# Optimization experiments

Measured on AMD Instinct MI355X. Metric: run time of the kernel, lower is better.

Reference implementation:

```python
import jax, jax.numpy as jnp
import numpy as np

# Winograd F(4x4, 3x3) transform matrices (wincnn convention, as in jiecaoyu/winograd)
BT = jnp.array([
    [4.,  0., -5.,  0., 1., 0.],
    [0., -4., -4.,  1., 1., 0.],
    [0.,  4., -4., -1., 1., 0.],
    [0., -2., -1.,  2., 1., 0.],
    [0.,  2., -1., -2., 1., 0.],
    [0.,  4.,  0., -5., 0., 1.]], dtype=jnp.float32)  # [6,6]
AT = jnp.array([
    [1., 1.,  1., 1.,  1., 0.],
    [0., 1., -1., 2., -2., 0.],
    [0., 1.,  1., 4.,  4., 0.],
    [0., 1., -1., 8., -8., 1.]], dtype=jnp.float32)  # [4,6]

KERNEL = 3
PAD = 1
GROUPS = 1
TILE_IN = 6   # input_tile_size
TILE_OUT = 4  # output_tile_size


def setup_inputs() -> dict:
    key = jax.random.key(0)
    k1, k2, k3 = jax.random.split(key, 3)
    N, Cin, H, W = 16, 64, 128, 128
    Cout = 64
    x = jax.random.normal(k1, (N, Cin, H, W), dtype=jnp.float32)
    # weight is stored in the Winograd (6x6 spectral) domain, as in the module
    weight = jax.random.normal(k2, (Cout, Cin // GROUPS, TILE_IN, TILE_IN), dtype=jnp.float32) * 0.01
    bias = jax.random.normal(k3, (Cout,), dtype=jnp.float32) * 0.01
    return {"x": x, "weight": weight, "bias": bias}


def reference(x, weight, bias):
    N, Cin, H0, W0 = x.shape
    Cout = weight.shape[0]
    g = GROUPS
    # conv padding
    x = jnp.pad(x, ((0, 0), (0, 0), (PAD, PAD), (PAD, PAD)))
    H = x.shape[2]
    out_w = H - KERNEL + 1
    # pad so output width is a multiple of the output tile size
    extra = (-out_w) % TILE_OUT
    if extra:
        x = jnp.pad(x, ((0, 0), (0, 0), (0, extra), (0, extra)))
    nt = (x.shape[2] - TILE_IN) // TILE_OUT + 1  # tiles per spatial dim
    # extract overlapping 6x6 tiles with stride 4 (the torch unfold)
    idx = jnp.arange(nt)[:, None] * TILE_OUT + jnp.arange(TILE_IN)[None, :]  # [nt,6]
    tiles = x[:, :, idx]                 # [N,C,nt,6,Wp]
    tiles = tiles[:, :, :, :, idx]       # [N,C,nt,6,nt,6]
    # input transform: V = BT @ d @ BT^T per tile -> [N,C,nt,nt,6,6]
    V = jnp.einsum('ai,ncpiqj,bj->ncpqab', BT, tiles, BT)
    # grouped spectral GEMM over input channels
    Vg = V.reshape(N, g, Cin // g, nt, nt, TILE_IN, TILE_IN)
    Wg = weight.reshape(g, Cout // g, Cin // g, TILE_IN, TILE_IN)
    M = jnp.einsum('goiab,ngipqab->ngopqab', Wg, Vg)
    M = M.reshape(N, Cout, nt, nt, TILE_IN, TILE_IN)
    # output transform: Y = AT @ M @ AT^T per tile -> [N,O,nt,nt,4,4]
    Y = jnp.einsum('xa,nopqab,yb->nopqxy', AT, M, AT)
    # stitch tiles back: [N,O,nt,4,nt,4] -> [N,O,nt*4,nt*4]
    y = Y.transpose(0, 1, 2, 4, 3, 5).reshape(N, Cout, nt * TILE_OUT, nt * TILE_OUT)
    y = y + bias[None, :, None, None]
    # crop the extra padding
    y = y[:, :, :out_w, :out_w]
    return y
```

## Files before the change

kernel.cpp:

```cpp
#include <hip/hip_runtime.h>
#include <stdint.h>

typedef __attribute__((ext_vector_type(4))) float f32x4;
typedef __attribute__((ext_vector_type(8))) short s16x8;

#define WB_BYTES 294912

__device__ __forceinline__ short f2bf(float f) {
    uint32_t u = __builtin_bit_cast(uint32_t, f);
    u = u + 0x7FFFu + ((u >> 16) & 1u);
    return (short)(u >> 16);
}

__global__ __launch_bounds__(256) void wtrans(const float* __restrict__ wf, short* __restrict__ wb) {
    int tid = blockIdx.x * 256 + threadIdx.x;
    const float* src = wf + tid * 36;
    float w[36];
#pragma unroll
    for (int i = 0; i < 9; i++) {
        f32x4 v = *(const f32x4*)(src + 4 * i);
        w[4*i+0] = v[0]; w[4*i+1] = v[1]; w[4*i+2] = v[2]; w[4*i+3] = v[3];
    }
#pragma unroll
    for (int ab = 0; ab < 36; ab++) wb[ab * 4096 + tid] = f2bf(w[ab]);
}

#define XS 343
__global__ __launch_bounds__(1024) void wino_fused(const float* __restrict__ x,
                                                   const short* __restrict__ wb,
                                                   const float* __restrict__ bias,
                                                   float* __restrict__ out) {
    __shared__ __align__(16) float SM[32768];
    float* X = SM;
    short* Vs = (short*)(SM + 32 * XS);
    float* P0 = SM;
    float* P1 = SM + 16384;

    int t = threadIdx.x;
    int lane = t & 63;
    int w = t >> 6;
    int cog = w >> 2;
    int grp = w & 3;
    int sh = grp >> 1;
    int bh = grp & 1;
    int lo = lane & 15;
    int kq = lane >> 4;

    int b = blockIdx.x;
    int n = b >> 6;
    int sb = b & 63;
    int p0_ = (sb >> 3) * 4;
    int q0_ = (sb & 7) * 4;
    const float* xb = x + (size_t)n * 64 * 16384;
    int row0 = 4 * p0_ - 1;
    int col0a = 4 * q0_ - 4;

    int ci_t = t & 31;
    int tl_t = (t >> 5) & 15;
    int s2_t = t >> 9;
    int tp = tl_t >> 2, tq = tl_t & 3;

    f32x4 acc[9];
#pragma unroll
    for (int i = 0; i < 9; i++) acc[i] = (f32x4){0.f, 0.f, 0.f, 0.f};

#pragma unroll
    for (int r = 0; r < 2; r++) {
#pragma unroll
        for (int i = 0; i < 4; i++) {
            int s = i * 1024 + t;
            if (s < 3456) {
                int cis = s / 108;
                int rs = s - cis * 108;
                int row = rs / 6;
                int c4 = rs - row * 6;
                int gr = row0 + row;
                int gc = col0a + 4 * c4;
                float v0 = 0.f, v1 = 0.f, v2 = 0.f, v3 = 0.f;
                if ((unsigned)gr < 128u) {
                    const float* rowp = xb + (size_t)((r * 32 + cis) * 128 + gr) * 128;
                    if (gc >= 0 && gc + 3 < 128) {
                        f32x4 v = *(const f32x4*)(rowp + gc);
                        v0 = v[0]; v1 = v[1]; v2 = v[2]; v3 = v[3];
                    } else {
                        if ((unsigned)(gc + 0) < 128u) v0 = rowp[gc + 0];
                        if ((unsigned)(gc + 1) < 128u) v1 = rowp[gc + 1];
                        if ((unsigned)(gc + 2) < 128u) v2 = rowp[gc + 2];
                        if ((unsigned)(gc + 3) < 128u) v3 = rowp[gc + 3];
                    }
                }
                int base = cis * XS + row * 18;
                int cl = 4 * c4 - 3;
                if ((unsigned)(cl + 0) < 18u) X[base + cl + 0] = v0;
                if ((unsigned)(cl + 1) < 18u) X[base + cl + 1] = v1;
                if ((unsigned)(cl + 2) < 18u) X[base + cl + 2] = v2;
                if ((unsigned)(cl + 3) < 18u) X[base + cl + 3] = v3;
            }
        }
        __syncthreads();

        {
            const float* Xb = X + ci_t * XS + (4 * tp) * 18 + 4 * tq;
            float Ua[3][6];
#pragma unroll
            for (int c = 0; c < 6; c++) {
                if (s2_t == 0) {
                    float m0 = Xb[0 * 18 + c], m1 = Xb[1 * 18 + c], m2 = Xb[2 * 18 + c];
                    float m3 = Xb[3 * 18 + c], m4 = Xb[4 * 18 + c];
                    float e = fmaf(-4.f, m2, m4);
                    float f = fmaf(-4.f, m1, m3);
                    Ua[0][c] = fmaf(4.f, m0 - m2, m4 - m2);
                    Ua[1][c] = e + f;
                    Ua[2][c] = e - f;
                } else {
                    float m1 = Xb[1 * 18 + c], m2 = Xb[2 * 18 + c];
                    float m3 = Xb[3 * 18 + c], m4 = Xb[4 * 18 + c], m5 = Xb[5 * 18 + c];
                    float g = m4 - m2, h = m3 - m1;
                    Ua[0][c] = fmaf(2.f, h, g);
                    Ua[1][c] = fmaf(-2.f, h, g);
                    Ua[2][c] = fmaf(4.f, m1 - m3, m5 - m3);
                }
            }
            short* vb = Vs + tl_t * 32 + ci_t;
#pragma unroll
            for (int ar = 0; ar < 3; ar++) {
                float m0 = Ua[ar][0], m1 = Ua[ar][1], m2 = Ua[ar][2];
                float m3 = Ua[ar][3], m4 = Ua[ar][4], m5 = Ua[ar][5];
                float e = fmaf(-4.f, m2, m4);
                float f = fmaf(-4.f, m1, m3);
                float g = m4 - m2;
                float h = m3 - m1;
                int abb = (s2_t * 3 + ar) * 6;
                vb[(abb + 0) * 512] = f2bf(fmaf(4.f, m0 - m2, g));
                vb[(abb + 1) * 512] = f2bf(e + f);
                vb[(abb + 2) * 512] = f2bf(e - f);
                vb[(abb + 3) * 512] = f2bf(fmaf(2.f, h, g));
                vb[(abb + 4) * 512] = f2bf(fmaf(-2.f, h, g));
                vb[(abb + 5) * 512] = f2bf(fmaf(4.f, m1 - m3, m5 - m3));
            }
        }
        __syncthreads();

        {
            const short* wb_base = wb + (cog * 16 + lo) * 64 + r * 32 + kq * 8;
            const short* v_base = Vs + lo * 32 + kq * 8;
#pragma unroll
            for (int ar = 0; ar < 3; ar++) {
#pragma unroll
                for (int br = 0; br < 3; br++) {
                    int ab = (3 * sh + ar) * 6 + (3 * bh + br);
                    s16x8 a0 = *(const s16x8*)(wb_base + ab * 4096);
                    s16x8 b0 = *(const s16x8*)(v_base + ab * 512);
                    acc[ar * 3 + br] = __builtin_amdgcn_mfma_f32_16x16x32_bf16(a0, b0, acc[ar * 3 + br], 0, 0, 0);
                }
            }
        }
    }

    __syncthreads();
    int p = p0_ + (lo >> 2);
    int q = q0_ + (lo & 3);
    float* Pown = (sh == 0) ? P0 : P1;

    if (bh == 0) {
#pragma unroll
        for (int rr = 0; rr < 4; rr++) {
            float z[4][3];
#pragma unroll
            for (int br = 0; br < 3; br++) {
                float ma = acc[br][rr], mb = acc[3 + br][rr], mc = acc[6 + br][rr];
                if (sh == 0) {
                    float s1 = mb + mc, d1 = mb - mc;
                    z[0][br] = ma + s1; z[1][br] = d1; z[2][br] = s1; z[3][br] = d1;
                } else {
                    float sv = ma + mb, dv = ma - mb;
                    z[0][br] = sv; z[1][br] = 2.f * dv; z[2][br] = 4.f * sv;
                    z[3][br] = fmaf(8.f, dv, mc);
                }
            }
#pragma unroll
            for (int xr = 0; xr < 4; xr++) {
                float s1 = z[xr][1] + z[xr][2], d1 = z[xr][1] - z[xr][2];
                f32x4 y;
                y[0] = z[xr][0] + s1; y[1] = d1; y[2] = s1; y[3] = d1;
                *(f32x4*)&Pown[cog * 4096 + (rr * 4 + xr) * 256 + lane * 4] = y;
            }
        }
    }
    __syncthreads();
    if (bh == 1) {
#pragma unroll
        for (int rr = 0; rr < 4; rr++) {
            float z[4][3];
#pragma unroll
            for (int br = 0; br < 3; br++) {
                float ma = acc[br][rr], mb = acc[3 + br][rr], mc = acc[6 + br][rr];
                if (sh == 0) {
                    float s1 = mb + mc, d1 = mb - mc;
                    z[0][br] = ma + s1; z[1][br] = d1; z[2][br] = s1; z[3][br] = d1;
                } else {
                    float sv = ma + mb, dv = ma - mb;
                    z[0][br] = sv; z[1][br] = 2.f * dv; z[2][br] = 4.f * sv;
                    z[3][br] = fmaf(8.f, dv, mc);
                }
            }
#pragma unroll
            for (int xr = 0; xr < 4; xr++) {
                float s2 = z[xr][0] + z[xr][1], d2 = z[xr][0] - z[xr][1];
                f32x4 y;
                y[0] = s2; y[1] = 2.f * d2; y[2] = 4.f * s2;
                y[3] = fmaf(8.f, d2, z[xr][2]);
                float* pp = &Pown[cog * 4096 + (rr * 4 + xr) * 256 + lane * 4];
                f32x4 old = *(const f32x4*)pp;
                *(f32x4*)pp = old + y;
            }
        }
    }
    __syncthreads();
    {
        int rr = grp;
        int co = cog * 16 + kq * 4 + rr;
        float bv = bias[co];
        float* ob = out + ((size_t)(n * 64 + co) * 128 + 4 * p) * 128 + 4 * q;
#pragma unroll
        for (int xr = 0; xr < 4; xr++) {
            int idx = cog * 4096 + (rr * 4 + xr) * 256 + lane * 4;
            f32x4 a0 = *(const f32x4*)&P0[idx];
            f32x4 a1 = *(const f32x4*)&P1[idx];
            f32x4 y;
            y[0] = a0[0] + a1[0] + bv;
            y[1] = a0[1] + a1[1] + bv;
            y[2] = a0[2] + a1[2] + bv;
            y[3] = a0[3] + a1[3] + bv;
            *(f32x4*)(ob + xr * 128) = y;
        }
    }
}

extern "C" void kernel_launch(void* const* d_in, const int* in_sizes, int n_in,
                              void* d_out, int out_size, void* d_ws, size_t ws_size,
                              hipStream_t stream) {
    const float* x    = (const float*)d_in[0];
    const float* wf   = (const float*)d_in[1];
    const float* bias = (const float*)d_in[2];
    float* out = (float*)d_out;

    if (ws_size < WB_BYTES) return;
    short* wb = (short*)d_ws;

    wtrans<<<16, 256, 0, stream>>>(wf, wb);
    wino_fused<<<1024, 1024, 0, stream>>>(x, wb, bias, out);
}
```

Before: 185.9 us.

## Make Winograd kernel persistent over four tiles with register-prefetched input loads

After: 224.1 us. +20.6%, slower.

```diff
diff --git a/kernel.cpp b/kernel.cpp
--- a/kernel.cpp
+++ b/kernel.cpp
@@ -2,6 +2,7 @@
 #include <stdint.h>
 
 typedef __attribute__((ext_vector_type(4))) float f32x4;
+typedef __attribute__((ext_vector_type(2))) float f32x2;
 typedef __attribute__((ext_vector_type(8))) short s16x8;
 
 #define WB_BYTES 294912
@@ -12,6 +13,12 @@
     return (short)(u >> 16);
 }
 
+__device__ __forceinline__ f32x4 load4u(const float* p) {
+    f32x4 v;
+    __builtin_memcpy(&v, p, 16);
+    return v;
+}
+
 __global__ __launch_bounds__(256) void wtrans(const float* __restrict__ wf, short* __restrict__ wb) {
     int tid = blockIdx.x * 256 + threadIdx.x;
     const float* src = wf + tid * 36;
@@ -25,14 +32,15 @@
     for (int ab = 0; ab < 36; ab++) wb[ab * 4096 + tid] = f2bf(w[ab]);
 }
 
-#define XS 343
+#define XCI 440
 __global__ __launch_bounds__(1024) void wino_fused(const float* __restrict__ x,
                                                    const short* __restrict__ wb,
                                                    const float* __restrict__ bias,
                                                    float* __restrict__ out) {
-    __shared__ __align__(16) float SM[32768];
-    float* X = SM;
-    short* Vs = (short*)(SM + 32 * XS);
+    __shared__ __align__(16) float SM[39680];
+    float* X0 = SM;
+    float* X1 = SM + 14080;
+    short* Vs = (short*)(SM + 28160);
     float* P0 = SM;
     float* P1 = SM + 16384;
 
@@ -46,194 +54,233 @@
     int lo = lane & 15;
     int kq = lane >> 4;
 
-    int b = blockIdx.x;
-    int n = b >> 6;
-    int sb = b & 63;
-    int p0_ = (sb >> 3) * 4;
-    int q0_ = (sb & 7) * 4;
-    const float* xb = x + (size_t)n * 64 * 16384;
-    int row0 = 4 * p0_ - 1;
-    int col0a = 4 * q0_ - 4;
-
     int ci_t = t & 31;
     int tl_t = (t >> 5) & 15;
     int s2_t = t >> 9;
     int tp = tl_t >> 2, tq = tl_t & 3;
 
+    int tci[4], trow[4], tc4[4];
+#pragma unroll
+    for (int i = 0; i < 4; i++) {
+        int s = i * 1024 + t;
+        int ci = s / 108;
+        int rem = s - ci * 108;
+        int row = rem / 6;
+        tci[i] = ci; trow[i] = row; tc4[i] = rem - row * 6;
+    }
+    bool v3 = t < 384;
+
+    float bv = bias[cog * 16 + kq * 4 + grp];
+
     f32x4 acc[9];
 #pragma unroll
     for (int i = 0; i < 9; i++) acc[i] = (f32x4){0.f, 0.f, 0.f, 0.f};
 
-#pragma unroll
-    for (int r = 0; r < 2; r++) {
+    f32x4 L[4];
+
+    auto issueLoads = [&](int vb, int r) {
+        int n = vb >> 6, sb = vb & 63;
+        int row0 = (sb >> 3) * 16 - 1;
+        int gc0 = (sb & 7) * 16 - 1;
+        const float* xb = x + (size_t)n * 64 * 16384;
 #pragma unroll
         for (int i = 0; i < 4; i++) {
-            int s = i * 1024 + t;
-            if (s < 3456) {
-                int cis = s / 108;
-                int rs = s - cis * 108;
-                int row = rs / 6;
-                int c4 = rs - row * 6;
-                int gr = row0 + row;
-                int gc = col0a + 4 * c4;
-                float v0 = 0.f, v1 = 0.f, v2 = 0.f, v3 = 0.f;
+            if (i < 3 || v3) {
+                int gr = row0 + trow[i];
+                int gc = gc0 + 4 * tc4[i];
+                f32x4 v = (f32x4){0.f, 0.f, 0.f, 0.f};
                 if ((unsigned)gr < 128u) {
-                    const float* rowp = xb + (size_t)((r * 32 + cis) * 128 + gr) * 128;
-                    if (gc >= 0 && gc + 3 < 128) {
-                        f32x4 v = *(const f32x4*)(rowp + gc);
-                        v0 = v[0]; v1 = v[1]; v2 = v[2]; v3 = v[3];
+                    const float* rowp = xb + (size_t)((r * 32 + tci[i]) * 128 + gr) * 128;
+                    if (gc >= 0 && gc <= 124) {
+                        v = load4u(rowp + gc);
                     } else {
-                        if ((unsigned)(gc + 0) < 128u) v0 = rowp[gc + 0];
-                        if ((unsigned)(gc + 1) < 128u) v1 = rowp[gc + 1];
-                        if ((unsigned)(gc + 2) < 128u) v2 = rowp[gc + 2];
-                        if ((unsigned)(gc + 3) < 128u) v3 = rowp[gc + 3];
+                        if ((unsigned)(gc + 0) < 128u) v[0] = rowp[gc + 0];
+                        if ((unsigned)(gc + 1) < 128u) v[1] = rowp[gc + 1];
+                        if ((unsigned)(gc + 2) < 128u) v[2] = rowp[gc + 2];
+                        if ((unsigned)(gc + 3) < 128u) v[3] = rowp[gc + 3];
                     }
                 }
-                int base = cis * XS + row * 18;
-                int cl = 4 * c4 - 3;
-                if ((unsigned)(cl + 0) < 18u) X[base + cl + 0] = v0;
-                if ((unsigned)(cl + 1) < 18u) X[base + cl + 1] = v1;
-                if ((unsigned)(cl + 2) < 18u) X[base + cl + 2] = v2;
-                if ((unsigned)(cl + 3) < 18u) X[base + cl + 3] = v3;
-            }
-        }
-        __syncthreads();
-
+                L[i] = v;
+            }
+        }
+    };
+
+    auto writeX = [&](float* Xb) {
+#pragma unroll
+        for (int i = 0; i < 4; i++) {
+            if (i < 3 || v3)
+                *(f32x4*)&Xb[tci[i] * XCI + trow[i] * 24 + tc4[i] * 4] = L[i];
+        }
+    };
+
+    auto transform = [&](const float* Xbuf) {
+        const float* Xb = Xbuf + ci_t * XCI + tp * 96 + tq * 4;
+        f32x4 ra[5]; f32x2 rb[5];
+#pragma unroll
+        for (int k = 0; k < 5; k++) {
+            int off = (s2_t + k) * 24;
+            ra[k] = *(const f32x4*)(Xb + off);
+            rb[k] = *(const f32x2*)(Xb + off + 4);
+        }
+        float Ua[3][6];
+#pragma unroll
+        for (int c = 0; c < 6; c++) {
+            float e0 = (c < 4) ? ra[0][c] : rb[0][c - 4];
+            float e1 = (c < 4) ? ra[1][c] : rb[1][c - 4];
+            float e2 = (c < 4) ? ra[2][c] : rb[2][c - 4];
+            float e3 = (c < 4) ? ra[3][c] : rb[3][c - 4];
+            float e4 = (c < 4) ? ra[4][c] : rb[4][c - 4];
+            if (s2_t == 0) {
+                float e = fmaf(-4.f, e2, e4);
+                float f = fmaf(-4.f, e1, e3);
+                Ua[0][c] = fmaf(4.f, e0 - e2, e4 - e2);
+                Ua[1][c] = e + f;
+                Ua[2][c] = e - f;
+            } else {
+                float g = e3 - e1;
+                float h = e2 - e0;
+                Ua[0][c] = fmaf(2.f, h, g);
+                Ua[1][c] = fmaf(-2.f, h, g);
+                Ua[2][c] = fmaf(4.f, e0 - e2, e4 - e2);
+            }
+        }
+        short* vb = Vs + tl_t * 40 + ci_t;
+#pragma unroll
+        for (int ar = 0; ar < 3; ar++) {
+            float m0 = Ua[ar][0], m1 = Ua[ar][1], m2 = Ua[ar][2];
+            float m3 = Ua[ar][3], m4 = Ua[ar][4], m5 = Ua[ar][5];
+            float e = fmaf(-4.f, m2, m4);
+            float f = fmaf(-4.f, m1, m3);
+            float g = m4 - m2;
+            float h = m3 - m1;
+            int base = (s2_t * 3 + ar) * 6;
+            vb[(base + 0) * 640] = f2bf(fmaf(4.f, m0 - m2, g));
+            vb[(base + 1) * 640] = f2bf(e + f);
+            vb[(base + 2) * 640] = f2bf(e - f);
+            vb[(base + 3) * 640] = f2bf(fmaf(2.f, h, g));
+            vb[(base + 4) * 640] = f2bf(fmaf(-2.f, h, g));
+            vb[(base + 5) * 640] = f2bf(fmaf(4.f, m1 - m3, m5 - m3));
+        }
+    };
+
+    auto gemmStep = [&](int r) {
+        const short* wb_base = wb + (cog * 16 + lo) * 64 + r * 32 + kq * 8;
+        const short* v_base = Vs + lo * 40 + kq * 8;
+#pragma unroll
+        for (int ar = 0; ar < 3; ar++) {
+#pragma unroll
+            for (int br = 0; br < 3; br++) {
+                int ab = (3 * sh + ar) * 6 + 3 * bh + br;
+                s16x8 a0 = *(const s16x8*)(wb_base + ab * 4096);
+                s16x8 b0 = *(const s16x8*)(v_base + ab * 640);
+                acc[ar * 3 + br] = __builtin_amdgcn_mfma_f32_16x16x32_bf16(a0, b0, acc[ar * 3 + br], 0, 0, 0);
+            }
+        }
+    };
+
+    int vb0 = blockIdx.x * 4;
+    issueLoads(vb0, 0);
+
+    for (int it = 0; it < 4; ++it) {
+        int vb = vb0 + it;
+        int n = vb >> 6, sb = vb & 63;
+        int p0_ = (sb >> 3) * 4;
+        int q0_ = (sb & 7) * 4;
+
+        writeX(X0);
+        __syncthreads();
+        issueLoads(vb, 1);
+        transform(X0);
+        writeX(X1);
+        __syncthreads();
+        gemmStep(0);
+        __syncthreads();
+        transform(X1);
+        __syncthreads();
+        gemmStep(1);
+        __syncthreads();
+
+        if (it < 3) issueLoads(vb + 1, 0);
+
+        int p = p0_ + (lo >> 2);
+        int q = q0_ + (lo & 3);
+        float* Pown = (sh == 0) ? P0 : P1;
+
+        if (bh == 0) {
+#pragma unroll
+            for (int rr = 0; rr < 4; rr++) {
+                float z[4][3];
+#pragma unroll
+                for (int br = 0; br < 3; br++) {
+                    float ma = acc[br][rr], mb = acc[3 + br][rr], mc = acc[6 + br][rr];
+                    if (sh == 0) {
+                        float s1 = mb + mc, d1 = mb - mc;
+                        z[0][br] = ma + s1; z[1][br] = d1; z[2][br] = s1; z[3][br] = d1;
+                    } else {
+                        float sv = ma + mb, dv = ma - mb;
+                        z[0][br] = sv; z[1][br] = 2.f * dv; z[2][br] = 4.f * sv;
+                        z[3][br] = fmaf(8.f, dv, mc);
+                    }
+                }
+#pragma unroll
+                for (int xr = 0; xr < 4; xr++) {
+                    float s1 = z[xr][1] + z[xr][2], d1 = z[xr][1] - z[xr][2];
+                    f32x4 y;
+                    y[0] = z[xr][0] + s1; y[1] = d1; y[2] = s1; y[3] = d1;
+                    *(f32x4*)&Pown[cog * 4096 + (rr * 4 + xr) * 256 + lane * 4] = y;
+                }
+            }
+        }
+        __syncthreads();
+        if (bh == 1) {
+#pragma unroll
+            for (int rr = 0; rr < 4; rr++) {
+                float z[4][3];
+#pragma unroll
+                for (int br = 0; br < 3; br++) {
+                    float ma = acc[br][rr], mb = acc[3 + br][rr], mc = acc[6 + br][rr];
+                    if (sh == 0) {
+                        float s1 = mb + mc, d1 = mb - mc;
+                        z[0][br] = ma + s1; z[1][br] = d1; z[2][br] = s1; z[3][br] = d1;
+                    } else {
+                        float sv = ma + mb, dv = ma - mb;
+                        z[0][br] = sv; z[1][br] = 2.f * dv; z[2][br] = 4.f * sv;
+                        z[3][br] = fmaf(8.f, dv, mc);
+                    }
+                }
+#pragma unroll
+                for (int xr = 0; xr < 4; xr++) {
+                    float s2 = z[xr][0] + z[xr][1], d2 = z[xr][0] - z[xr][1];
+                    f32x4 y;
+                    y[0] = s2; y[1] = 2.f * d2; y[2] = 4.f * s2;
+                    y[3] = fmaf(8.f, d2, z[xr][2]);
+                    float* pp = &Pown[cog * 4096 + (rr * 4 + xr) * 256 + lane * 4];
+                    f32x4 old = *(const f32x4*)pp;
+                    *(f32x4*)pp = old + y;
+                }
+            }
+        }
+        __syncthreads();
         {
-            const float* Xb = X + ci_t * XS + (4 * tp) * 18 + 4 * tq;
-            float Ua[3][6];
-#pragma unroll
-            for (int c = 0; c < 6; c++) {
-                if (s2_t == 0) {
-                    float m0 = Xb[0 * 18 + c], m1 = Xb[1 * 18 + c], m2 = Xb[2 * 18 + c];
-                    float m3 = Xb[3 * 18 + c], m4 = Xb[4 * 18 + c];
-                    float e = fmaf(-4.f, m2, m4);
-                    float f = fmaf(-4.f, m1, m3);
-                    Ua[0][c] = fmaf(4.f, m0 - m2, m4 - m2);
-                    Ua[1][c] = e + f;
-                    Ua[2][c] = e - f;
-                } else {
-                    float m1 = Xb[1 * 18 + c], m2 = Xb[2 * 18 + c];
-                    float m3 = Xb[3 * 18 + c], m4 = Xb[4 * 18 + c], m5 = Xb[5 * 18 + c];
-                    float g = m4 - m2, h = m3 - m1;
-                    Ua[0][c] = fmaf(2.f, h, g);
-                    Ua[1][c] = fmaf(-2.f, h, g);
-                    Ua[2][c] = fmaf(4.f, m1 - m3, m5 - m3);
-                }
-            }
-            short* vb = Vs + tl_t * 32 + ci_t;
-#pragma unroll
-            for (int ar = 0; ar < 3; ar++) {
-                float m0 = Ua[ar][0], m1 = Ua[ar][1], m2 = Ua[ar][2];
-                float m3 = Ua[ar][3], m4 = Ua[ar][4], m5 = Ua[ar][5];
-                float e = fmaf(-4.f, m2, m4);
-                float f = fmaf(-4.f, m1, m3);
-                float g = m4 - m2;
-                float h = m3 - m1;
-                int abb = (s2_t * 3 + ar) * 6;
-                vb[(abb + 0) * 512] = f2bf(fmaf(4.f, m0 - m2, g));
-                vb[(abb + 1) * 512] = f2bf(e + f);
-                vb[(abb + 2) * 512] = f2bf(e - f);
-                vb[(abb + 3) * 512] = f2bf(fmaf(2.f, h, g));
-                vb[(abb + 4) * 512] = f2bf(fmaf(-2.f, h, g));
-                vb[(abb + 5) * 512] = f2bf(fmaf(4.f, m1 - m3, m5 - m3));
-            }
-        }
-        __syncthreads();
-
-        {
-            const short* wb_base = wb + (cog * 16 + lo) * 64 + r * 32 + kq * 8;
-            const short* v_base = Vs + lo * 32 + kq * 8;
-#pragma unroll
-            for (int ar = 0; ar < 3; ar++) {
-#pragma unroll
-                for (int br = 0; br < 3; br++) {
-                    int ab = (3 * sh + ar) * 6 + (3 * bh + br);
-                    s16x8 a0 = *(const s16x8*)(wb_base + ab * 4096);
-                    s16x8 b0 = *(const s16x8*)(v_base + ab * 512);
-                    acc[ar * 3 + br] = __builtin_amdgcn_mfma_f32_16x16x32_bf16(a0, b0, acc[ar * 3 + br], 0, 0, 0);
-                }
-            }
-        }
-    }
-
-    __syncthreads();
-    int p = p0_ + (lo >> 2);
-    int q = q0_ + (lo & 3);
-    float* Pown = (sh == 0) ? P0 : P1;
-
-    if (bh == 0) {
-#pragma unroll
-        for (int rr = 0; rr < 4; rr++) {
-            float z[4][3];
-#pragma unroll
-            for (int br = 0; br < 3; br++) {
-                float ma = acc[br][rr], mb = acc[3 + br][rr], mc = acc[6 + br][rr];
-                if (sh == 0) {
-                    float s1 = mb + mc, d1 = mb - mc;
-                    z[0][br] = ma + s1; z[1][br] = d1; z[2][br] = s1; z[3][br] = d1;
-                } else {
-                    float sv = ma + mb, dv = ma - mb;
-                    z[0][br] = sv; z[1][br] = 2.f * dv; z[2][br] = 4.f * sv;
-                    z[3][br] = fmaf(8.f, dv, mc);
-                }
-            }
+            int rr = grp;
+            int co = cog * 16 + kq * 4 + rr;
+            float* ob = out + ((size_t)(n * 64 + co) * 128 + 4 * p) * 128 + 4 * q;
 #pragma unroll
             for (int xr = 0; xr < 4; xr++) {
-                float s1 = z[xr][1] + z[xr][2], d1 = z[xr][1] - z[xr][2];
+                int idx = cog * 4096 + (rr * 4 + xr) * 256 + lane * 4;
+                f32x4 a0 = *(const f32x4*)&P0[idx];
+                f32x4 a1 = *(const f32x4*)&P1[idx];
                 f32x4 y;
-                y[0] = z[xr][0] + s1; y[1] = d1; y[2] = s1; y[3] = d1;
-                *(f32x4*)&Pown[cog * 4096 + (rr * 4 + xr) * 256 + lane * 4] = y;
-            }
-        }
-    }
-    __syncthreads();
-    if (bh == 1) {
-#pragma unroll
-        for (int rr = 0; rr < 4; rr++) {
-            float z[4][3];
-#pragma unroll
-            for (int br = 0; br < 3; br++) {
-                float ma = acc[br][rr], mb = acc[3 + br][rr], mc = acc[6 + br][rr];
-                if (sh == 0) {
-                    float s1 = mb + mc, d1 = mb - mc;
-                    z[0][br] = ma + s1; z[1][br] = d1; z[2][br] = s1; z[3][br] = d1;
-                } else {
-                    float sv = ma + mb, dv = ma - mb;
-                    z[0][br] = sv; z[1][br] = 2.f * dv; z[2][br] = 4.f * sv;
-                    z[3][br] = fmaf(8.f, dv, mc);
-                }
-            }
-#pragma unroll
-            for (int xr = 0; xr < 4; xr++) {
-                float s2 = z[xr][0] + z[xr][1], d2 = z[xr][0] - z[xr][1];
-                f32x4 y;
-                y[0] = s2; y[1] = 2.f * d2; y[2] = 4.f * s2;
-                y[3] = fmaf(8.f, d2, z[xr][2]);
-                float* pp = &Pown[cog * 4096 + (rr * 4 + xr) * 256 + lane * 4];
-                f32x4 old = *(const f32x4*)pp;
-                *(f32x4*)pp = old + y;
-            }
-        }
-    }
-    __syncthreads();
-    {
-        int rr = grp;
-        int co = cog * 16 + kq * 4 + rr;
-        float bv = bias[co];
-        float* ob = out + ((size_t)(n * 64 + co) * 128 + 4 * p) * 128 + 4 * q;
-#pragma unroll
-        for (int xr = 0; xr < 4; xr++) {
-            int idx = cog * 4096 + (rr * 4 + xr) * 256 + lane * 4;
-            f32x4 a0 = *(const f32x4*)&P0[idx];
-            f32x4 a1 = *(const f32x4*)&P1[idx];
-            f32x4 y;
-            y[0] = a0[0] + a1[0] + bv;
-            y[1] = a0[1] + a1[1] + bv;
-            y[2] = a0[2] + a1[2] + bv;
-            y[3] = a0[3] + a1[3] + bv;
-            *(f32x4*)(ob + xr * 128) = y;
-        }
+                y[0] = a0[0] + a1[0] + bv;
+                y[1] = a0[1] + a1[1] + bv;
+                y[2] = a0[2] + a1[2] + bv;
+                y[3] = a0[3] + a1[3] + bv;
+                *(f32x4*)(ob + xr * 128) = y;
+            }
+        }
+#pragma unroll
+        for (int i = 0; i < 9; i++) acc[i] = (f32x4){0.f, 0.f, 0.f, 0.f};
+        if (it < 3) __syncthreads();
     }
 }
 
@@ -249,5 +296,5 @@
     short* wb = (short*)d_ws;
 
     wtrans<<<16, 256, 0, stream>>>(wf, wb);
-    wino_fused<<<1024, 1024, 0, stream>>>(x, wb, bias, out);
-}
+    wino_fused<<<256, 1024, 0, stream>>>(x, wb, bias, out);
+}
```
